# Kernel optimization log

Hardware: AMD Instinct MI355X
Metric: run time of the kernel (lower is better)

Reference implementation:

```python
import jax, jax.numpy as jnp
import numpy as np

NUM_LATENT = 1024
LATENT_DIM = 256
BETA = 0.25
N_TOKENS = 65536


def setup_inputs() -> dict:
    key = jax.random.key(0)
    k1, k2 = jax.random.split(key)
    latent_embedding = jax.random.normal(k1, (N_TOKENS, LATENT_DIM), dtype=jnp.float32)
    # torch.nn.init.uniform_(codebook, -1/num_latent, 1/num_latent)
    codebook = jax.random.uniform(
        k2, (NUM_LATENT, LATENT_DIM), dtype=jnp.float32,
        minval=-1.0 / NUM_LATENT, maxval=1.0 / NUM_LATENT)
    return {"latent_embedding": latent_embedding, "codebook": codebook}


def reference(latent_embedding, codebook):
    le_det = jax.lax.stop_gradient(latent_embedding)  # [N, D]
    # distances[n,k] = ||z_n||^2 + ||c_k||^2 - 2 z_n . c_k   (z detached, codebook NOT)
    distances = (jnp.sum(le_det ** 2, axis=1, keepdims=True)
                 + jnp.sum(codebook ** 2, axis=1)
                 - 2.0 * jnp.matmul(le_det, codebook.T))  # [N, K]
    encoding_inds = jnp.argmin(distances, axis=1)  # [N]
    # one_hot @ codebook == gather rows of codebook
    quantized_latents = codebook[encoding_inds]  # [N, D]
    num_latent = codebook.shape[0]
    commitment_loss = jnp.mean((jax.lax.stop_gradient(quantized_latents)
                                - latent_embedding) ** 2) * num_latent
    embedding_loss = jnp.mean((quantized_latents - le_det) ** 2) * num_latent
    vq_loss = embedding_loss + commitment_loss * BETA
    probs = jax.nn.softmax(-distances, axis=1)  # [N, K]
    probs = jnp.clip(jnp.mean(probs, axis=0, keepdims=True), 0.001, 0.999)  # [1, K]
    return (quantized_latents, codebook, probs, vq_loss)
```

## Files before the change

### kernel.cpp

```cpp
#include <hip/hip_runtime.h>

#define N_TOK 65536
#define DIM   256
#define K_CODES 1024
#define CB_OFF    16777216
#define PROBS_OFF (16777216 + 262144)
#define LOSS_OFF  (16777216 + 262144 + 1024)

typedef float  f32x4  __attribute__((ext_vector_type(4)));
typedef short  s16x8  __attribute__((ext_vector_type(8)));

__device__ __forceinline__ unsigned short f32_to_bf16(float x) {
    unsigned u = __float_as_uint(x);
    unsigned r = (u + 0x7FFFu + ((u >> 16) & 1u)) >> 16;
    return (unsigned short)r;
}

__global__ __launch_bounds__(512) void k_prep(const float* __restrict__ cb,
                                              float* __restrict__ c2,
                                              unsigned short* __restrict__ cbf) {
    const int g  = blockIdx.x;
    const int t  = threadIdx.x;
    const int wv = t >> 6;
    const int ln = t & 63;
    const int l15 = ln & 15, q = ln >> 4;

    const float* zp = cb + (size_t)(g * 16 + l15) * DIM + wv * 32 + q * 8;
    f32x4 z0 = *(const f32x4*)(zp);
    f32x4 z1 = *(const f32x4*)(zp + 4);
    s16x8 a;
    a[0] = (short)f32_to_bf16(z0[0]); a[1] = (short)f32_to_bf16(z0[1]);
    a[2] = (short)f32_to_bf16(z0[2]); a[3] = (short)f32_to_bf16(z0[3]);
    a[4] = (short)f32_to_bf16(z1[0]); a[5] = (short)f32_to_bf16(z1[1]);
    a[6] = (short)f32_to_bf16(z1[2]); a[7] = (short)f32_to_bf16(z1[3]);
    *(s16x8*)(cbf + (size_t)(g * 8 + wv) * 1024 + ln * 8) = a;

    float s = z0[0]*z0[0] + z0[1]*z0[1] + z0[2]*z0[2] + z0[3]*z0[3]
            + z1[0]*z1[0] + z1[1]*z1[1] + z1[2]*z1[2] + z1[3]*z1[3];
    s += __shfl_xor(s, 16, 64);
    s += __shfl_xor(s, 32, 64);
    __shared__ float c2p[8][16];
    if (q == 0) c2p[wv][l15] = s;
    __syncthreads();
    if (t < 16) {
        float acc = 0.f;
        #pragma unroll
        for (int ww = 0; ww < 8; ww++) acc += c2p[ww][t];
        c2[g * 16 + t] = acc;
    }
}

__global__ __launch_bounds__(512, 4) void k_main(const float* __restrict__ z,
                                                 const float* __restrict__ cb,
                                                 const unsigned short* __restrict__ cbf,
                                                 const float* __restrict__ c2,
                                                 float* __restrict__ out_q,
                                                 float* __restrict__ probs_part,
                                                 float* __restrict__ lossR,
                                                 int repmask) {
    const int t   = threadIdx.x;
    const int w   = t >> 6;
    const int ln  = t & 63;
    const int q   = ln >> 4;
    const int l15 = ln & 15;
    const int k0  = w * 128;
    const int n0  = blockIdx.x * 32;
    float* pp = probs_part + (blockIdx.x & repmask) * K_CODES;

    __shared__ unsigned short a_lds[16 * 64 * 8];
    __shared__ float z2s[32];
    __shared__ float redmin[8][32];
    __shared__ int   redidx[8][32];
    __shared__ float rede[8][32];
    __shared__ int   fidx[32];
    __shared__ float fU[32];

    if (t < 32) z2s[t] = 0.f;
    __syncthreads();

    #pragma unroll
    for (int rep = 0; rep < 2; rep++) {
        const int f   = t + rep * 512;
        const int md  = f >> 6;
        const int fl  = f & 63;
        const int row = ((md >> 3) * 16) + (fl & 15);
        const int dim = (md & 7) * 32 + (fl >> 4) * 8;
        const float* zp = z + (size_t)(n0 + row) * DIM + dim;
        f32x4 z0 = *(const f32x4*)(zp);
        f32x4 z1 = *(const f32x4*)(zp + 4);
        s16x8 a;
        a[0] = (short)f32_to_bf16(z0[0]); a[1] = (short)f32_to_bf16(z0[1]);
        a[2] = (short)f32_to_bf16(z0[2]); a[3] = (short)f32_to_bf16(z0[3]);
        a[4] = (short)f32_to_bf16(z1[0]); a[5] = (short)f32_to_bf16(z1[1]);
        a[6] = (short)f32_to_bf16(z1[2]); a[7] = (short)f32_to_bf16(z1[3]);
        *(s16x8*)(a_lds + (size_t)f * 8) = a;
        float s = z0[0]*z0[0] + z0[1]*z0[1] + z0[2]*z0[2] + z0[3]*z0[3]
                + z1[0]*z1[0] + z1[1]*z1[1] + z1[2]*z1[2] + z1[3]*z1[3];
        atomicAdd(&z2s[row], s);
    }
    __syncthreads();

    f32x4 acc[2][8];
    #pragma unroll
    for (int m = 0; m < 2; m++)
        #pragma unroll
        for (int nt = 0; nt < 8; nt++) { f32x4 zr = {0.f, 0.f, 0.f, 0.f}; acc[m][nt] = zr; }

    const unsigned short* bb = cbf + (size_t)(w * 8) * 8 * 1024 + ln * 8;

    #pragma unroll
    for (int ds = 0; ds < 8; ds++) {
        s16x8 a0 = *(const s16x8*)(a_lds + (size_t)((0 * 8 + ds) * 64 + ln) * 8);
        s16x8 a1 = *(const s16x8*)(a_lds + (size_t)((1 * 8 + ds) * 64 + ln) * 8);
        #pragma unroll
        for (int nt = 0; nt < 8; nt++) {
            s16x8 b = *(const s16x8*)(bb + (size_t)(nt * 8 + ds) * 1024);
            acc[0][nt] = __builtin_amdgcn_mfma_f32_16x16x32_bf16(a0, b, acc[0][nt], 0, 0, 0);
            acc[1][nt] = __builtin_amdgcn_mfma_f32_16x16x32_bf16(a1, b, acc[1][nt], 0, 0, 0);
        }
    }

    float c2v[8];
    #pragma unroll
    for (int nt = 0; nt < 8; nt++) c2v[nt] = c2[k0 + nt * 16 + l15];

    float lmin[2][4], lesum[2][4]; int lidx[2][4];
    #pragma unroll
    for (int m = 0; m < 2; m++)
        #pragma unroll
        for (int v = 0; v < 4; v++) { lmin[m][v] = 3.4e38f; lidx[m][v] = 0x7fffffff; lesum[m][v] = 0.f; }

    #pragma unroll
    for (int m = 0; m < 2; m++)
        #pragma unroll
        for (int nt = 0; nt < 8; nt++) {
            const int col = k0 + nt * 16 + l15;
            #pragma unroll
            for (int v = 0; v < 4; v++) {
                float s = c2v[nt] - 2.0f * acc[m][nt][v];
                if (s < lmin[m][v]) { lmin[m][v] = s; lidx[m][v] = col; }
                float e = __expf(-s);
                acc[m][nt][v] = e;
                lesum[m][v] += e;
            }
        }

    #pragma unroll
    for (int off = 1; off < 16; off <<= 1) {
        #pragma unroll
        for (int m = 0; m < 2; m++)
            #pragma unroll
            for (int v = 0; v < 4; v++) {
                float omin = __shfl_xor(lmin[m][v], off, 64);
                int   oidx = __shfl_xor(lidx[m][v], off, 64);
                float oes  = __shfl_xor(lesum[m][v], off, 64);
                if (omin < lmin[m][v] || (omin == lmin[m][v] && oidx < lidx[m][v])) {
                    lmin[m][v] = omin; lidx[m][v] = oidx;
                }
                lesum[m][v] += oes;
            }
    }

    if (l15 == 0) {
        #pragma unroll
        for (int m = 0; m < 2; m++)
            #pragma unroll
            for (int v = 0; v < 4; v++) {
                const int r = m * 16 + q * 4 + v;
                redmin[w][r] = lmin[m][v]; redidx[w][r] = lidx[m][v]; rede[w][r] = lesum[m][v];
            }
    }
    __syncthreads();
    float lossreg = 0.f;
    if (t < 32) {
        float bm = redmin[0][t]; int bi = redidx[0][t];
        float U  = rede[0][t];
        #pragma unroll
        for (int ww = 1; ww < 8; ww++) {
            float m2 = redmin[ww][t]; int i2 = redidx[ww][t];
            if (m2 < bm || (m2 == bm && i2 < bi)) { bm = m2; bi = i2; }
            U += rede[ww][t];
        }
        fidx[t] = bi; fU[t] = U;
        lossreg = z2s[t] + bm;
    }
    __syncthreads();

    float ps[8];
    #pragma unroll
    for (int nt = 0; nt < 8; nt++) ps[nt] = 0.f;
    #pragma unroll
    for (int m = 0; m < 2; m++)
        #pragma unroll
        for (int v = 0; v < 4; v++) {
            const float invU = 1.0f / fU[m * 16 + q * 4 + v];
            #pragma unroll
            for (int nt = 0; nt < 8; nt++) ps[nt] += acc[m][nt][v] * invU;
        }
    #pragma unroll
    for (int nt = 0; nt < 8; nt++) {
        ps[nt] += __shfl_xor(ps[nt], 16, 64);
        ps[nt] += __shfl_xor(ps[nt], 32, 64);
    }
    #pragma unroll
    for (int j = 0; j < 2; j++) {
        const int nt = q * 2 + j;
        atomicAdd(&pp[k0 + nt * 16 + l15], ps[nt]);
    }

    #pragma unroll
    for (int i = 0; i < 4; i++) {
        const int r  = w * 4 + i;
        const int am = fidx[r];
        f32x4 qv = *(const f32x4*)(cb + (size_t)am * DIM + ln * 4);
        *(f32x4*)(out_q + (size_t)(n0 + r) * DIM + ln * 4) = qv;
    }

    if (w == 0) {
        #pragma unroll
        for (int off = 32; off; off >>= 1) lossreg += __shfl_down(lossreg, off, 64);
        if (ln == 0) atomicAdd(&lossR[blockIdx.x & 63], lossreg);
    }
}

__global__ __launch_bounds__(256) void k_fin(const float* __restrict__ cb,
                                             const float* __restrict__ probs_part,
                                             const float* __restrict__ lossR,
                                             float* __restrict__ out,
                                             int R, int nLoss) {
    const int g = blockIdx.x * 256 + threadIdx.x;
    out[CB_OFF + g] = cb[g];
    if (g < K_CODES) {
        float acc = 0.f;
        for (int r = 0; r < R; r++) acc += probs_part[r * K_CODES + g];
        float p = acc * (1.0f / 65536.0f);
        p = fminf(fmaxf(p, 0.001f), 0.999f);
        out[PROBS_OFF + g] = p;
    }
    if (g == 0) {
        float ls = 0.f;
        for (int r = 0; r < nLoss; r++) ls += lossR[r];
        out[LOSS_OFF] = ls * (1280.0f / 16777216.0f);
    }
}

extern "C" void kernel_launch(void* const* d_in, const int* in_sizes, int n_in,
                              void* d_out, int out_size, void* d_ws, size_t ws_size,
                              hipStream_t stream) {
    (void)in_sizes; (void)n_in; (void)out_size;
    const float* z  = (const float*)d_in[0];
    const float* cb = (const float*)d_in[1];
    float* out = (float*)d_out;

    float* c2 = (float*)d_ws;
    unsigned short* cbf = (unsigned short*)(out + CB_OFF);

    float *probs_part, *lossR;
    int R = 64, nLoss;
    while (R > 1 && ws_size < (size_t)(1024 + 64 + R * 1024) * 4) R >>= 1;
    if (ws_size >= (size_t)(1024 + 64 + R * 1024) * 4) {
        lossR      = c2 + 1024;
        probs_part = lossR + 64;
        nLoss = 64;
        hipMemsetAsync(lossR, 0, (size_t)(64 + R * 1024) * 4, stream);
    } else {
        probs_part = out + PROBS_OFF;
        lossR      = out + LOSS_OFF;
        R = 1; nLoss = 1;
        hipMemsetAsync(out + PROBS_OFF, 0, (size_t)(K_CODES + 1) * 4, stream);
    }

    k_prep<<<dim3(K_CODES / 16), dim3(512), 0, stream>>>(cb, c2, cbf);
    k_main<<<dim3(N_TOK / 32), dim3(512), 0, stream>>>(z, cb, cbf, c2, out, probs_part,
                                                       lossR, R - 1);
    k_fin<<<dim3(262144 / 256), dim3(256), 0, stream>>>(cb, probs_part, lossR, out, R, nLoss);
}
```

Baseline: 218.5 us.

## Enlarge row tile to 64 with 1024-thread blocks and pack argmin into keys

Each block of k_main now covers 64 tokens with 16 waves, and each wave handles 64 codes. Every codebook fragment loaded is reused across four A tiles. The -c2/2 bias is folded into the MFMA accumulator init, and the argmin is done as a max over packed order-preserving keys that carry the column index in the low 10 bits. The probs/loss zeroing and the codebook copy move into k_prep, and the bf16 codebook can live in workspace. The risks are register pressure at 1024 threads with launch bounds of 4, and truncated distance bits, which can change tie-breaking and the loss value.

```diff
diff --git a/kernel.cpp b/kernel.cpp
--- a/kernel.cpp
+++ b/kernel.cpp
@@ -6,6 +6,7 @@
 #define CB_OFF    16777216
 #define PROBS_OFF (16777216 + 262144)
 #define LOSS_OFF  (16777216 + 262144 + 1024)
+#define TM 64
 
 typedef float  f32x4  __attribute__((ext_vector_type(4)));
 typedef short  s16x8  __attribute__((ext_vector_type(8)));
@@ -15,10 +16,23 @@
     unsigned r = (u + 0x7FFFu + ((u >> 16) & 1u)) >> 16;
     return (unsigned short)r;
 }
+__device__ __forceinline__ unsigned fkey(float a) {
+    unsigned u = __float_as_uint(a);
+    unsigned m = (unsigned)(((int)u) >> 31);
+    return u ^ (m | 0x80000000u);
+}
+__device__ __forceinline__ float fkey_inv(unsigned k) {
+    unsigned u = (k & 0x80000000u) ? (k ^ 0x80000000u) : ~k;
+    return __uint_as_float(u);
+}
 
 __global__ __launch_bounds__(512) void k_prep(const float* __restrict__ cb,
                                               float* __restrict__ c2,
-                                              unsigned short* __restrict__ cbf) {
+                                              unsigned short* __restrict__ cbf,
+                                              float* __restrict__ probs_part,
+                                              float* __restrict__ lossR,
+                                              float* __restrict__ outcb,
+                                              int zcount, int nloss, int docopy) {
     const int g  = blockIdx.x;
     const int t  = threadIdx.x;
     const int wv = t >> 6;
@@ -41,6 +55,16 @@
     s += __shfl_xor(s, 32, 64);
     __shared__ float c2p[8][16];
     if (q == 0) c2p[wv][l15] = s;
+
+    const int base = g * 512 + t;
+    if (base < nloss) lossR[base] = 0.f;
+    if (base < zcount) probs_part[base] = 0.f;
+    if (base + 32768 < zcount) probs_part[base + 32768] = 0.f;
+    if (docopy) {
+        #pragma unroll
+        for (int i = 0; i < 8; i++) outcb[base + i * 32768] = cb[base + i * 32768];
+    }
+
     __syncthreads();
     if (t < 16) {
         float acc = 0.f;
@@ -50,41 +74,38 @@
     }
 }
 
-__global__ __launch_bounds__(512, 4) void k_main(const float* __restrict__ z,
-                                                 const float* __restrict__ cb,
-                                                 const unsigned short* __restrict__ cbf,
-                                                 const float* __restrict__ c2,
-                                                 float* __restrict__ out_q,
-                                                 float* __restrict__ probs_part,
-                                                 float* __restrict__ lossR,
-                                                 int repmask) {
+__global__ __launch_bounds__(1024, 4) void k_main(const float* __restrict__ z,
+                                                  const float* __restrict__ cb,
+                                                  const unsigned short* __restrict__ cbf,
+                                                  const float* __restrict__ c2,
+                                                  float* __restrict__ out_q,
+                                                  float* __restrict__ probs_part,
+                                                  float* __restrict__ lossR,
+                                                  int repmask) {
     const int t   = threadIdx.x;
     const int w   = t >> 6;
     const int ln  = t & 63;
     const int q   = ln >> 4;
     const int l15 = ln & 15;
-    const int k0  = w * 128;
-    const int n0  = blockIdx.x * 32;
+    const int k0  = w * 64;
+    const int n0  = blockIdx.x * TM;
     float* pp = probs_part + (blockIdx.x & repmask) * K_CODES;
 
-    __shared__ unsigned short a_lds[16 * 64 * 8];
-    __shared__ float z2s[32];
-    __shared__ float redmin[8][32];
-    __shared__ int   redidx[8][32];
-    __shared__ float rede[8][32];
-    __shared__ int   fidx[32];
-    __shared__ float fU[32];
-
-    if (t < 32) z2s[t] = 0.f;
-    __syncthreads();
+    __shared__ unsigned short a_lds[32 * 64 * 8];
+    __shared__ float    z2p[32][16];
+    __shared__ unsigned kred[16][64];
+    __shared__ float    ered[16][64];
+    __shared__ int   fidx[64];
+    __shared__ float fU[64];
 
     #pragma unroll
     for (int rep = 0; rep < 2; rep++) {
-        const int f   = t + rep * 512;
-        const int md  = f >> 6;
-        const int fl  = f & 63;
-        const int row = ((md >> 3) * 16) + (fl & 15);
-        const int dim = (md & 7) * 32 + (fl >> 4) * 8;
+        const int f   = t + rep * 1024;
+        const int md  = w + rep * 16;
+        const int m   = md >> 3;
+        const int dsv = md & 7;
+        const int row = m * 16 + l15;
+        const int dim = dsv * 32 + q * 8;
         const float* zp = z + (size_t)(n0 + row) * DIM + dim;
         f32x4 z0 = *(const f32x4*)(zp);
         f32x4 z1 = *(const f32x4*)(zp + 4);
@@ -96,50 +117,60 @@
         *(s16x8*)(a_lds + (size_t)f * 8) = a;
         float s = z0[0]*z0[0] + z0[1]*z0[1] + z0[2]*z0[2] + z0[3]*z0[3]
                 + z1[0]*z1[0] + z1[1]*z1[1] + z1[2]*z1[2] + z1[3]*z1[3];
-        atomicAdd(&z2s[row], s);
-    }
+        s += __shfl_xor(s, 16, 64);
+        s += __shfl_xor(s, 32, 64);
+        if (q == 0) z2p[md][l15] = s;
+    }
+
+    float c2v[4];
+    #pragma unroll
+    for (int nt = 0; nt < 4; nt++) c2v[nt] = c2[k0 + nt * 16 + l15];
+    f32x4 acc[4][4];
+    #pragma unroll
+    for (int m = 0; m < 4; m++)
+        #pragma unroll
+        for (int nt = 0; nt < 4; nt++) {
+            const float iv = -0.5f * c2v[nt];
+            f32x4 v4 = {iv, iv, iv, iv};
+            acc[m][nt] = v4;
+        }
+
     __syncthreads();
 
-    f32x4 acc[2][8];
-    #pragma unroll
-    for (int m = 0; m < 2; m++)
-        #pragma unroll
-        for (int nt = 0; nt < 8; nt++) { f32x4 zr = {0.f, 0.f, 0.f, 0.f}; acc[m][nt] = zr; }
-
-    const unsigned short* bb = cbf + (size_t)(w * 8) * 8 * 1024 + ln * 8;
-
+    const unsigned short* bb = cbf + (size_t)(w * 4) * 8 * 1024 + ln * 8;
     #pragma unroll
     for (int ds = 0; ds < 8; ds++) {
-        s16x8 a0 = *(const s16x8*)(a_lds + (size_t)((0 * 8 + ds) * 64 + ln) * 8);
-        s16x8 a1 = *(const s16x8*)(a_lds + (size_t)((1 * 8 + ds) * 64 + ln) * 8);
-        #pragma unroll
-        for (int nt = 0; nt < 8; nt++) {
+        s16x8 af[4];
+        #pragma unroll
+        for (int m = 0; m < 4; m++)
+            af[m] = *(const s16x8*)(a_lds + (size_t)((m * 8 + ds) * 64 + ln) * 8);
+        #pragma unroll
+        for (int nt = 0; nt < 4; nt++) {
             s16x8 b = *(const s16x8*)(bb + (size_t)(nt * 8 + ds) * 1024);
-            acc[0][nt] = __builtin_amdgcn_mfma_f32_16x16x32_bf16(a0, b, acc[0][nt], 0, 0, 0);
-            acc[1][nt] = __builtin_amdgcn_mfma_f32_16x16x32_bf16(a1, b, acc[1][nt], 0, 0, 0);
-        }
-    }
-
-    float c2v[8];
-    #pragma unroll
-    for (int nt = 0; nt < 8; nt++) c2v[nt] = c2[k0 + nt * 16 + l15];
-
-    float lmin[2][4], lesum[2][4]; int lidx[2][4];
-    #pragma unroll
-    for (int m = 0; m < 2; m++)
-        #pragma unroll
-        for (int v = 0; v < 4; v++) { lmin[m][v] = 3.4e38f; lidx[m][v] = 0x7fffffff; lesum[m][v] = 0.f; }
-
-    #pragma unroll
-    for (int m = 0; m < 2; m++)
-        #pragma unroll
-        for (int nt = 0; nt < 8; nt++) {
-            const int col = k0 + nt * 16 + l15;
+            #pragma unroll
+            for (int m = 0; m < 4; m++)
+                acc[m][nt] = __builtin_amdgcn_mfma_f32_16x16x32_bf16(af[m], b, acc[m][nt], 0, 0, 0);
+        }
+    }
+
+    unsigned lkey[4][4];
+    float    lesum[4][4];
+    #pragma unroll
+    for (int m = 0; m < 4; m++)
+        #pragma unroll
+        for (int v = 0; v < 4; v++) { lkey[m][v] = 0u; lesum[m][v] = 0.f; }
+
+    #pragma unroll
+    for (int m = 0; m < 4; m++)
+        #pragma unroll
+        for (int nt = 0; nt < 4; nt++) {
+            const unsigned colc = 1023u - (unsigned)(k0 + nt * 16 + l15);
             #pragma unroll
             for (int v = 0; v < 4; v++) {
-                float s = c2v[nt] - 2.0f * acc[m][nt][v];
-                if (s < lmin[m][v]) { lmin[m][v] = s; lidx[m][v] = col; }
-                float e = __expf(-s);
+                float a = acc[m][nt][v];
+                unsigned key = (fkey(a) & 0xFFFFFC00u) | colc;
+                lkey[m][v] = max(lkey[m][v], key);
+                float e = __expf(a + a);
                 acc[m][nt][v] = e;
                 lesum[m][v] += e;
             }
@@ -148,65 +179,62 @@
     #pragma unroll
     for (int off = 1; off < 16; off <<= 1) {
         #pragma unroll
-        for (int m = 0; m < 2; m++)
+        for (int m = 0; m < 4; m++)
             #pragma unroll
             for (int v = 0; v < 4; v++) {
-                float omin = __shfl_xor(lmin[m][v], off, 64);
-                int   oidx = __shfl_xor(lidx[m][v], off, 64);
-                float oes  = __shfl_xor(lesum[m][v], off, 64);
-                if (omin < lmin[m][v] || (omin == lmin[m][v] && oidx < lidx[m][v])) {
-                    lmin[m][v] = omin; lidx[m][v] = oidx;
-                }
-                lesum[m][v] += oes;
+                unsigned ok = (unsigned)__shfl_xor((int)lkey[m][v], off, 64);
+                float    oe = __shfl_xor(lesum[m][v], off, 64);
+                lkey[m][v] = max(lkey[m][v], ok);
+                lesum[m][v] += oe;
             }
     }
 
     if (l15 == 0) {
         #pragma unroll
-        for (int m = 0; m < 2; m++)
+        for (int m = 0; m < 4; m++)
             #pragma unroll
             for (int v = 0; v < 4; v++) {
                 const int r = m * 16 + q * 4 + v;
-                redmin[w][r] = lmin[m][v]; redidx[w][r] = lidx[m][v]; rede[w][r] = lesum[m][v];
+                kred[w][r] = lkey[m][v]; ered[w][r] = lesum[m][v];
             }
     }
     __syncthreads();
     float lossreg = 0.f;
-    if (t < 32) {
-        float bm = redmin[0][t]; int bi = redidx[0][t];
-        float U  = rede[0][t];
-        #pragma unroll
-        for (int ww = 1; ww < 8; ww++) {
-            float m2 = redmin[ww][t]; int i2 = redidx[ww][t];
-            if (m2 < bm || (m2 == bm && i2 < bi)) { bm = m2; bi = i2; }
-            U += rede[ww][t];
-        }
-        fidx[t] = bi; fU[t] = U;
-        lossreg = z2s[t] + bm;
+    if (t < 64) {
+        unsigned bk = kred[0][t];
+        float U = ered[0][t];
+        #pragma unroll
+        for (int ww = 1; ww < 16; ww++) {
+            bk = max(bk, kred[ww][t]);
+            U += ered[ww][t];
+        }
+        fidx[t] = 1023 - (int)(bk & 1023u);
+        fU[t] = U;
+        float a_rec = fkey_inv(bk);
+        float z2 = 0.f;
+        #pragma unroll
+        for (int ds = 0; ds < 8; ds++) z2 += z2p[(t >> 4) * 8 + ds][t & 15];
+        lossreg = z2 - 2.0f * a_rec;
     }
     __syncthreads();
 
-    float ps[8];
-    #pragma unroll
-    for (int nt = 0; nt < 8; nt++) ps[nt] = 0.f;
-    #pragma unroll
-    for (int m = 0; m < 2; m++)
+    float ps[4];
+    #pragma unroll
+    for (int nt = 0; nt < 4; nt++) ps[nt] = 0.f;
+    #pragma unroll
+    for (int m = 0; m < 4; m++)
         #pragma unroll
         for (int v = 0; v < 4; v++) {
             const float invU = 1.0f / fU[m * 16 + q * 4 + v];
             #pragma unroll
-            for (int nt = 0; nt < 8; nt++) ps[nt] += acc[m][nt][v] * invU;
-        }
-    #pragma unroll
-    for (int nt = 0; nt < 8; nt++) {
+            for (int nt = 0; nt < 4; nt++) ps[nt] += acc[m][nt][v] * invU;
+        }
+    #pragma unroll
+    for (int nt = 0; nt < 4; nt++) {
         ps[nt] += __shfl_xor(ps[nt], 16, 64);
         ps[nt] += __shfl_xor(ps[nt], 32, 64);
     }
-    #pragma unroll
-    for (int j = 0; j < 2; j++) {
-        const int nt = q * 2 + j;
-        atomicAdd(&pp[k0 + nt * 16 + l15], ps[nt]);
-    }
+    atomicAdd(&pp[k0 + q * 16 + l15], ps[q]);
 
     #pragma unroll
     for (int i = 0; i < 4; i++) {
@@ -227,13 +255,22 @@
                                              const float* __restrict__ probs_part,
                                              const float* __restrict__ lossR,
                                              float* __restrict__ out,
-                                             int R, int nLoss) {
+                                             int R, int nLoss, int docopy) {
     const int g = blockIdx.x * 256 + threadIdx.x;
-    out[CB_OFF + g] = cb[g];
+    if (docopy && g < 262144) out[CB_OFF + g] = cb[g];
     if (g < K_CODES) {
-        float acc = 0.f;
-        for (int r = 0; r < R; r++) acc += probs_part[r * K_CODES + g];
-        float p = acc * (1.0f / 65536.0f);
+        float a0 = 0.f, a1 = 0.f, a2 = 0.f, a3 = 0.f;
+        if (R >= 4) {
+            for (int r = 0; r < R; r += 4) {
+                a0 += probs_part[(r + 0) * K_CODES + g];
+                a1 += probs_part[(r + 1) * K_CODES + g];
+                a2 += probs_part[(r + 2) * K_CODES + g];
+                a3 += probs_part[(r + 3) * K_CODES + g];
+            }
+        } else {
+            for (int r = 0; r < R; r++) a0 += probs_part[r * K_CODES + g];
+        }
+        float p = (a0 + a1 + a2 + a3) * (1.0f / 65536.0f);
         p = fminf(fmaxf(p, 0.001f), 0.999f);
         out[PROBS_OFF + g] = p;
     }
@@ -253,25 +290,36 @@
     float* out = (float*)d_out;
 
     float* c2 = (float*)d_ws;
-    unsigned short* cbf = (unsigned short*)(out + CB_OFF);
 
     float *probs_part, *lossR;
-    int R = 64, nLoss;
-    while (R > 1 && ws_size < (size_t)(1024 + 64 + R * 1024) * 4) R >>= 1;
-    if (ws_size >= (size_t)(1024 + 64 + R * 1024) * 4) {
+    int R, nLoss;
+    size_t used = 1024 * 4;
+    auto fits = [&](int r) { return ws_size >= used + (size_t)(64 + r * 1024) * 4; };
+    if      (fits(64)) R = 64;
+    else if (fits(16)) R = 16;
+    else if (fits(4))  R = 4;
+    else               R = 0;
+    if (R) {
         lossR      = c2 + 1024;
         probs_part = lossR + 64;
         nLoss = 64;
-        hipMemsetAsync(lossR, 0, (size_t)(64 + R * 1024) * 4, stream);
+        used += (size_t)(64 + R * 1024) * 4;
     } else {
         probs_part = out + PROBS_OFF;
         lossR      = out + LOSS_OFF;
         R = 1; nLoss = 1;
-        hipMemsetAsync(out + PROBS_OFF, 0, (size_t)(K_CODES + 1) * 4, stream);
-    }
-
-    k_prep<<<dim3(K_CODES / 16), dim3(512), 0, stream>>>(cb, c2, cbf);
-    k_main<<<dim3(N_TOK / 32), dim3(512), 0, stream>>>(z, cb, cbf, c2, out, probs_part,
-                                                       lossR, R - 1);
-    k_fin<<<dim3(262144 / 256), dim3(256), 0, stream>>>(cb, probs_part, lossR, out, R, nLoss);
-}
+    }
+
+    unsigned short* cbf;
+    int cbf_in_ws = (ws_size >= used + (size_t)K_CODES * DIM * 2);
+    if (cbf_in_ws) cbf = (unsigned short*)((char*)d_ws + used);
+    else           cbf = (unsigned short*)(out + CB_OFF);
+
+    k_prep<<<dim3(64), dim3(512), 0, stream>>>(cb, c2, cbf, probs_part, lossR,
+                                               out + CB_OFF, R * 1024, nLoss, cbf_in_ws);
+    k_main<<<dim3(N_TOK / TM), dim3(1024), 0, stream>>>(z, cb, cbf, c2, out, probs_part,
+                                                        lossR, R - 1);
+    const int fin_blocks = cbf_in_ws ? 4 : 1024;
+    k_fin<<<dim3(fin_blocks), dim3(256), 0, stream>>>(cb, probs_part, lossR, out,
+                                                      R, nLoss, !cbf_in_ws);
+}
```

Result: faster. 208.1 us (-4.8%).
